# Kernel tuning notes

Hardware: AMD Instinct MI355X
Metric: run time of the kernel (lower is better)

The kernel has to match this reference:

```python
import jax, jax.numpy as jnp
import numpy as np

R = 2.0            # distance exponent
Q = 1.0            # activation exponent
SPECIFICITY = 1.0  # c in exp(-c * dist)
BETA = 3.0         # lateral competition exponent
TEMP_COMP = 1.0    # ClusterCompetition temperature
TEMP_WTA = 0.1     # SoftWTA temperature
PHI = 1.5          # association scaling
NEG_INF = -1e30

B, C, D = 1024, 512, 256


def setup_inputs() -> dict:
    key = jax.random.key(0)
    k1, k2, k3, k4, k5 = jax.random.split(key, 5)
    inp = jax.random.normal(k1, (B, D), dtype=jnp.float32)
    w_dist = jax.random.normal(k2, (C, D), dtype=jnp.float32)      # cluster centers
    attn = jax.random.uniform(k3, (D,), dtype=jnp.float32)         # dim-wise attention (>=0)
    w_assoc = jax.random.normal(k4, (C, 2), dtype=jnp.float32)     # association weights
    mask = jax.random.randint(k5, (C,), 0, 2, dtype=jnp.int32)     # recruited-cluster mask
    return {"inp": inp, "w_dist": w_dist, "attn": attn, "w_assoc": w_assoc, "mask": mask}


def reference(inp, w_dist, attn, w_assoc, mask):
    m = mask.astype(inp.dtype)                       # [C] 0/1 recruited gate
    # Distance: per-dim |x - w|^r for every (item, cluster) pair -> [B, C, D]
    dim_dist = jnp.abs(inp[:, None, :] - w_dist[None, :, :]) ** R
    # DimWiseAttention: sum-to-one constrained attention over dims
    a = attn / jnp.sum(attn)
    # ClusterActivation: H_j = exp(-c * (sum_d a_d * dist_d)^(q/r)) -> [B, C]
    wdist = jnp.einsum('bcd,d->bc', dim_dist, a)
    H = jnp.exp(-SPECIFICITY * wdist ** (Q / R))
    clusters_actv = H * m                            # MaskNonRecruit
    nonzero = m > 0
    # ClusterCompetition: softmax over recruited clusters of actv^beta (temp-scaled),
    # re-weighting each cluster's own activation.
    comp_logits = jnp.where(nonzero, BETA * jnp.log(H) / TEMP_COMP, NEG_INF)
    p_comp = jax.nn.softmax(comp_logits, axis=-1)
    competed = p_comp * clusters_actv                # [B, C]
    # SoftWTA: plain temperature softmax over recruited clusters, same re-weighting.
    wta_logits = jnp.where(nonzero, competed / TEMP_WTA, NEG_INF)
    p_wta = jax.nn.softmax(wta_logits, axis=-1)
    softwta = p_wta * competed                       # [B, C]
    # Classification: Phi-scaled linear readout to 2 classes.
    y_pred = PHI * (softwta @ w_assoc)               # [B, 2]
    return y_pred
```

## Files before the change

### kernel.cpp

```cpp
#include <hip/hip_runtime.h>
#include <math.h>

#define BN 1024
#define CN 512
#define DN 256
#define TM 128
#define TN 64
#define KZ 32
#define NZ (DN / KZ)

#define XS_OFF 0
#define R_OFF  (BN * DN)
#define Q_OFF  (R_OFF + BN)
#define PD_OFF (Q_OFF + CN)

__launch_bounds__(256, 4)
__global__ void prep_kernel(const float* __restrict__ inp, const float* __restrict__ wd,
                            const float* __restrict__ attn, float* __restrict__ ws) {
    __shared__ float red[4];
    float* xs = ws + XS_OFF;
    float* r  = ws + R_OFF;
    float* q  = ws + Q_OFF;

    const int tid  = threadIdx.x;
    const int lane = tid & 63;
    const int blk  = blockIdx.x;

    float av = attn[tid];
    float s = av;
    #pragma unroll
    for (int off = 32; off > 0; off >>= 1) s += __shfl_xor(s, off);
    if (lane == 0) red[tid >> 6] = s;
    __syncthreads();
    const float a = av / (red[0] + red[1] + red[2] + red[3]);

    float c;
    if (blk < BN) {
        const float x = inp[blk * DN + tid];
        xs[blk * DN + tid] = a * x;
        c = a * x * x;
    } else {
        const float w = wd[(blk - BN) * DN + tid];
        c = a * w * w;
    }
    #pragma unroll
    for (int off = 32; off > 0; off >>= 1) c += __shfl_xor(c, off);
    __syncthreads();
    if (lane == 0) red[tid >> 6] = c;
    __syncthreads();
    if (tid == 0) {
        const float tot = red[0] + red[1] + red[2] + red[3];
        if (blk < BN) r[blk] = tot; else q[blk - BN] = tot;
    }
}

__launch_bounds__(256, 2)
__global__ void dist_kernel(const float* __restrict__ ws_ro, const float* __restrict__ wd,
                            float* __restrict__ ws) {
    __shared__ __align__(16) float aT[TM * KZ];
    __shared__ __align__(16) float bT[TN * KZ];

    const float* xs = ws_ro + XS_OFF;
    float* pdot = ws + PD_OFF + (size_t)blockIdx.z * BN * CN;

    const int tid = threadIdx.x;
    const int m0 = blockIdx.x * TM;
    const int n0 = blockIdx.y * TN;
    const int k0 = blockIdx.z * KZ;

    {
        const int row = tid >> 1;
        const int g0  = (tid & 1) * 4;
        const int sw  = (row >> 3) & 7;
        const float* src = &xs[(m0 + row) * DN + k0 + 4 * g0];
        float4* dst = (float4*)&aT[row * KZ];
        #pragma unroll
        for (int j = 0; j < 4; ++j)
            dst[(g0 + j) ^ sw] = *(const float4*)&src[4 * j];
    }
    {
        const int row = tid >> 2;
        const int g0  = (tid & 3) * 2;
        const int sw  = (row >> 3) & 7;
        const float* src = &wd[(n0 + row) * DN + k0 + 4 * g0];
        float4* dst = (float4*)&bT[row * KZ];
        #pragma unroll
        for (int j = 0; j < 2; ++j)
            dst[(g0 + j) ^ sw] = *(const float4*)&src[4 * j];
    }
    __syncthreads();

    const int tr = tid & 15;
    const int tc = tid >> 4;
    const int swa = tr & 7;
    const int swb = (tc >> 1) & 7;
    float acc[8][4] = {};

    #pragma unroll
    for (int k4 = 0; k4 < KZ / 4; ++k4) {
        float4 av[8], bv[4];
        #pragma unroll
        for (int i = 0; i < 8; ++i)
            av[i] = ((const float4*)&aT[(8 * tr + i) * KZ])[k4 ^ swa];
        #pragma unroll
        for (int j = 0; j < 4; ++j)
            bv[j] = ((const float4*)&bT[(4 * tc + j) * KZ])[k4 ^ swb];
        #pragma unroll
        for (int i = 0; i < 8; ++i)
            #pragma unroll
            for (int j = 0; j < 4; ++j) {
                float t = fmaf(av[i].x, bv[j].x, acc[i][j]);
                t = fmaf(av[i].y, bv[j].y, t);
                t = fmaf(av[i].z, bv[j].z, t);
                acc[i][j] = fmaf(av[i].w, bv[j].w, t);
            }
    }

    #pragma unroll
    for (int i = 0; i < 8; ++i) {
        float4 o = {acc[i][0], acc[i][1], acc[i][2], acc[i][3]};
        *(float4*)&pdot[(m0 + 8 * tr + i) * CN + n0 + 4 * tc] = o;
    }
}

#define NEG_INF_F (-1e30f)

__device__ __forceinline__ float waveMax(float v) {
    #pragma unroll
    for (int off = 32; off > 0; off >>= 1) v = fmaxf(v, __shfl_xor(v, off));
    return v;
}
__device__ __forceinline__ float waveSum(float v) {
    #pragma unroll
    for (int off = 32; off > 0; off >>= 1) v += __shfl_xor(v, off);
    return v;
}

__launch_bounds__(256, 2)
__global__ void finish_kernel(const float* __restrict__ ws, const int* __restrict__ mask,
                              const float* __restrict__ w_assoc, float* __restrict__ y) {
    const float* r    = ws + R_OFF;
    const float* q    = ws + Q_OFF;
    const float* pdot = ws + PD_OFF;

    const int tid  = threadIdx.x;
    const int lane = tid & 63;
    const int b    = blockIdx.x * 4 + (tid >> 6);
    const int cb   = lane * 8;

    float dot[8] = {};
    #pragma unroll
    for (int z = 0; z < NZ; ++z) {
        const float* pz = &pdot[(size_t)z * BN * CN + b * CN + cb];
        #pragma unroll
        for (int s4 = 0; s4 < 2; ++s4) {
            const float4 v = *(const float4*)&pz[4 * s4];
            dot[4 * s4 + 0] += v.x; dot[4 * s4 + 1] += v.y;
            dot[4 * s4 + 2] += v.z; dot[4 * s4 + 3] += v.w;
        }
    }
    const float rb = r[b];
    const float4 q0 = *(const float4*)&q[cb];
    const float4 q1 = *(const float4*)&q[cb + 4];
    const float qv[8] = {q0.x, q0.y, q0.z, q0.w, q1.x, q1.y, q1.z, q1.w};

    float t[8];
    #pragma unroll
    for (int j = 0; j < 8; ++j)
        t[j] = sqrtf(fmaxf(rb + qv[j] - 2.0f * dot[j], 0.0f));

    const int4 mm0 = *(const int4*)&mask[cb];
    const int4 mm1 = *(const int4*)&mask[cb + 4];
    const bool rec[8] = {mm0.x > 0, mm0.y > 0, mm0.z > 0, mm0.w > 0,
                         mm1.x > 0, mm1.y > 0, mm1.z > 0, mm1.w > 0};

    float l1[8], lmax = NEG_INF_F;
    #pragma unroll
    for (int j = 0; j < 8; ++j) { l1[j] = rec[j] ? (-3.0f * t[j]) : NEG_INF_F; lmax = fmaxf(lmax, l1[j]); }
    const float mx1 = waveMax(lmax);
    float e1[8], lsum = 0.f;
    #pragma unroll
    for (int j = 0; j < 8; ++j) { e1[j] = rec[j] ? expf(l1[j] - mx1) : 0.f; lsum += e1[j]; }
    const float inv_s1 = 1.0f / waveSum(lsum);

    float competed[8];
    #pragma unroll
    for (int j = 0; j < 8; ++j) competed[j] = e1[j] * inv_s1 * expf(-t[j]);

    float l2[8]; lmax = NEG_INF_F;
    #pragma unroll
    for (int j = 0; j < 8; ++j) { l2[j] = rec[j] ? (competed[j] * 10.0f) : NEG_INF_F; lmax = fmaxf(lmax, l2[j]); }
    const float mx2 = waveMax(lmax);
    float e2[8]; lsum = 0.f;
    #pragma unroll
    for (int j = 0; j < 8; ++j) { e2[j] = rec[j] ? expf(l2[j] - mx2) : 0.f; lsum += e2[j]; }
    const float inv_s2 = 1.0f / waveSum(lsum);

    float y0 = 0.f, y1 = 0.f;
    #pragma unroll
    for (int p = 0; p < 4; ++p) {
        const float4 wa = *(const float4*)&w_assoc[2 * cb + 4 * p];
        const float sw0 = e2[2 * p + 0] * inv_s2 * competed[2 * p + 0];
        const float sw1 = e2[2 * p + 1] * inv_s2 * competed[2 * p + 1];
        y0 = fmaf(sw0, wa.x, y0); y1 = fmaf(sw0, wa.y, y1);
        y0 = fmaf(sw1, wa.z, y0); y1 = fmaf(sw1, wa.w, y1);
    }
    y0 = waveSum(y0);
    y1 = waveSum(y1);
    if (lane == 0) {
        float2 o = {1.5f * y0, 1.5f * y1};
        *(float2*)&y[b * 2] = o;
    }
}

extern "C" void kernel_launch(void* const* d_in, const int* in_sizes, int n_in,
                              void* d_out, int out_size, void* d_ws, size_t ws_size,
                              hipStream_t stream) {
    const float* inp     = (const float*)d_in[0];
    const float* w_dist  = (const float*)d_in[1];
    const float* attn    = (const float*)d_in[2];
    const float* w_assoc = (const float*)d_in[3];
    const int*   mask    = (const int*)d_in[4];
    float* out = (float*)d_out;
    float* ws  = (float*)d_ws;

    prep_kernel<<<BN + CN, 256, 0, stream>>>(inp, w_dist, attn, ws);
    dim3 gA(BN / TM, CN / TN, NZ);
    dist_kernel<<<gA, 256, 0, stream>>>(ws, w_dist, ws);
    finish_kernel<<<BN / 4, 256, 0, stream>>>(ws, mask, w_assoc, out);
}
```

Before: 82.94 us.

## Fuse distance GEMM and softmax readout into one kernel with in-block k-split reduction

Replaces the tiled split-K dist kernel, which wrote 8 partial dot-product planes to global workspace, and the separate finish kernel with a single fused kernel. Each 512-thread block handles 4 batch rows. Each wave computes a K-slice of the dot products against all 512 clusters, reading w_dist straight from global memory. The partials are reduced in shared memory and the softmax readout runs in place. This removes the large partial-sum round trip and one launch, but gives up LDS tiling: w_dist is re-read from global/L2 by every block, with strided per-lane accesses and low data reuse.

```diff
diff --git a/kernel.cpp b/kernel.cpp
--- a/kernel.cpp
+++ b/kernel.cpp
@@ -4,15 +4,13 @@
 #define BN 1024
 #define CN 512
 #define DN 256
-#define TM 128
-#define TN 64
-#define KZ 32
-#define NZ (DN / KZ)
+#define ROWS 4
+#define WAVES 8
+#define KC (DN / WAVES)
 
 #define XS_OFF 0
 #define R_OFF  (BN * DN)
 #define Q_OFF  (R_OFF + BN)
-#define PD_OFF (Q_OFF + CN)
 
 __launch_bounds__(256, 4)
 __global__ void prep_kernel(const float* __restrict__ inp, const float* __restrict__ wd,
@@ -54,75 +52,6 @@
     }
 }
 
-__launch_bounds__(256, 2)
-__global__ void dist_kernel(const float* __restrict__ ws_ro, const float* __restrict__ wd,
-                            float* __restrict__ ws) {
-    __shared__ __align__(16) float aT[TM * KZ];
-    __shared__ __align__(16) float bT[TN * KZ];
-
-    const float* xs = ws_ro + XS_OFF;
-    float* pdot = ws + PD_OFF + (size_t)blockIdx.z * BN * CN;
-
-    const int tid = threadIdx.x;
-    const int m0 = blockIdx.x * TM;
-    const int n0 = blockIdx.y * TN;
-    const int k0 = blockIdx.z * KZ;
-
-    {
-        const int row = tid >> 1;
-        const int g0  = (tid & 1) * 4;
-        const int sw  = (row >> 3) & 7;
-        const float* src = &xs[(m0 + row) * DN + k0 + 4 * g0];
-        float4* dst = (float4*)&aT[row * KZ];
-        #pragma unroll
-        for (int j = 0; j < 4; ++j)
-            dst[(g0 + j) ^ sw] = *(const float4*)&src[4 * j];
-    }
-    {
-        const int row = tid >> 2;
-        const int g0  = (tid & 3) * 2;
-        const int sw  = (row >> 3) & 7;
-        const float* src = &wd[(n0 + row) * DN + k0 + 4 * g0];
-        float4* dst = (float4*)&bT[row * KZ];
-        #pragma unroll
-        for (int j = 0; j < 2; ++j)
-            dst[(g0 + j) ^ sw] = *(const float4*)&src[4 * j];
-    }
-    __syncthreads();
-
-    const int tr = tid & 15;
-    const int tc = tid >> 4;
-    const int swa = tr & 7;
-    const int swb = (tc >> 1) & 7;
-    float acc[8][4] = {};
-
-    #pragma unroll
-    for (int k4 = 0; k4 < KZ / 4; ++k4) {
-        float4 av[8], bv[4];
-        #pragma unroll
-        for (int i = 0; i < 8; ++i)
-            av[i] = ((const float4*)&aT[(8 * tr + i) * KZ])[k4 ^ swa];
-        #pragma unroll
-        for (int j = 0; j < 4; ++j)
-            bv[j] = ((const float4*)&bT[(4 * tc + j) * KZ])[k4 ^ swb];
-        #pragma unroll
-        for (int i = 0; i < 8; ++i)
-            #pragma unroll
-            for (int j = 0; j < 4; ++j) {
-                float t = fmaf(av[i].x, bv[j].x, acc[i][j]);
-                t = fmaf(av[i].y, bv[j].y, t);
-                t = fmaf(av[i].z, bv[j].z, t);
-                acc[i][j] = fmaf(av[i].w, bv[j].w, t);
-            }
-    }
-
-    #pragma unroll
-    for (int i = 0; i < 8; ++i) {
-        float4 o = {acc[i][0], acc[i][1], acc[i][2], acc[i][3]};
-        *(float4*)&pdot[(m0 + 8 * tr + i) * CN + n0 + 4 * tc] = o;
-    }
-}
-
 #define NEG_INF_F (-1e30f)
 
 __device__ __forceinline__ float waveMax(float v) {
@@ -136,80 +65,113 @@
     return v;
 }
 
-__launch_bounds__(256, 2)
-__global__ void finish_kernel(const float* __restrict__ ws, const int* __restrict__ mask,
-                              const float* __restrict__ w_assoc, float* __restrict__ y) {
-    const float* r    = ws + R_OFF;
-    const float* q    = ws + Q_OFF;
-    const float* pdot = ws + PD_OFF;
+__launch_bounds__(512, 1)
+__global__ void fused_kernel(const float* __restrict__ ws, const float* __restrict__ wd,
+                             const int* __restrict__ mask, const float* __restrict__ w_assoc,
+                             float* __restrict__ y) {
+    __shared__ float red[WAVES * 32 * 64];
 
     const int tid  = threadIdx.x;
     const int lane = tid & 63;
-    const int b    = blockIdx.x * 4 + (tid >> 6);
-    const int cb   = lane * 8;
+    const int wz   = __builtin_amdgcn_readfirstlane(tid >> 6);
+    const int b0   = blockIdx.x * ROWS;
+    const int kbase = wz * KC;
 
-    float dot[8] = {};
+    const float* xs = ws + XS_OFF;
+
+    const float* wp[8];
     #pragma unroll
-    for (int z = 0; z < NZ; ++z) {
-        const float* pz = &pdot[(size_t)z * BN * CN + b * CN + cb];
+    for (int j = 0; j < 8; ++j)
+        wp[j] = wd + (size_t)(lane + 64 * j) * DN + kbase;
+
+    float acc[ROWS][8] = {};
+
+    #pragma unroll
+    for (int k4 = 0; k4 < KC / 4; ++k4) {
+        float4 xv[ROWS];
         #pragma unroll
-        for (int s4 = 0; s4 < 2; ++s4) {
-            const float4 v = *(const float4*)&pz[4 * s4];
-            dot[4 * s4 + 0] += v.x; dot[4 * s4 + 1] += v.y;
-            dot[4 * s4 + 2] += v.z; dot[4 * s4 + 3] += v.w;
+        for (int rr = 0; rr < ROWS; ++rr) {
+            const int idx = __builtin_amdgcn_readfirstlane((b0 + rr) * DN + kbase + 4 * k4);
+            xv[rr] = *(const float4*)&xs[idx];
+        }
+        #pragma unroll
+        for (int j = 0; j < 8; ++j) {
+            const float4 w4 = *(const float4*)(wp[j] + 4 * k4);
+            #pragma unroll
+            for (int rr = 0; rr < ROWS; ++rr) {
+                float t = fmaf(xv[rr].x, w4.x, acc[rr][j]);
+                t = fmaf(xv[rr].y, w4.y, t);
+                t = fmaf(xv[rr].z, w4.z, t);
+                acc[rr][j] = fmaf(xv[rr].w, w4.w, t);
+            }
         }
     }
-    const float rb = r[b];
-    const float4 q0 = *(const float4*)&q[cb];
-    const float4 q1 = *(const float4*)&q[cb + 4];
-    const float qv[8] = {q0.x, q0.y, q0.z, q0.w, q1.x, q1.y, q1.z, q1.w};
 
-    float t[8];
     #pragma unroll
-    for (int j = 0; j < 8; ++j)
-        t[j] = sqrtf(fmaxf(rb + qv[j] - 2.0f * dot[j], 0.0f));
+    for (int rr = 0; rr < ROWS; ++rr)
+        #pragma unroll
+        for (int j = 0; j < 8; ++j)
+            red[(wz * 32 + rr * 8 + j) * 64 + lane] = acc[rr][j];
+    __syncthreads();
 
-    const int4 mm0 = *(const int4*)&mask[cb];
-    const int4 mm1 = *(const int4*)&mask[cb + 4];
-    const bool rec[8] = {mm0.x > 0, mm0.y > 0, mm0.z > 0, mm0.w > 0,
-                         mm1.x > 0, mm1.y > 0, mm1.z > 0, mm1.w > 0};
+    if (wz < ROWS) {
+        const int rr = wz;
 
-    float l1[8], lmax = NEG_INF_F;
-    #pragma unroll
-    for (int j = 0; j < 8; ++j) { l1[j] = rec[j] ? (-3.0f * t[j]) : NEG_INF_F; lmax = fmaxf(lmax, l1[j]); }
-    const float mx1 = waveMax(lmax);
-    float e1[8], lsum = 0.f;
-    #pragma unroll
-    for (int j = 0; j < 8; ++j) { e1[j] = rec[j] ? expf(l1[j] - mx1) : 0.f; lsum += e1[j]; }
-    const float inv_s1 = 1.0f / waveSum(lsum);
+        float dot[8] = {};
+        #pragma unroll
+        for (int z = 0; z < WAVES; ++z)
+            #pragma unroll
+            for (int j = 0; j < 8; ++j)
+                dot[j] += red[(z * 32 + rr * 8 + j) * 64 + lane];
 
-    float competed[8];
-    #pragma unroll
-    for (int j = 0; j < 8; ++j) competed[j] = e1[j] * inv_s1 * expf(-t[j]);
+        const float rb = ws[R_OFF + b0 + rr];
 
-    float l2[8]; lmax = NEG_INF_F;
-    #pragma unroll
-    for (int j = 0; j < 8; ++j) { l2[j] = rec[j] ? (competed[j] * 10.0f) : NEG_INF_F; lmax = fmaxf(lmax, l2[j]); }
-    const float mx2 = waveMax(lmax);
-    float e2[8]; lsum = 0.f;
-    #pragma unroll
-    for (int j = 0; j < 8; ++j) { e2[j] = rec[j] ? expf(l2[j] - mx2) : 0.f; lsum += e2[j]; }
-    const float inv_s2 = 1.0f / waveSum(lsum);
+        float t[8]; bool rec[8];
+        #pragma unroll
+        for (int j = 0; j < 8; ++j) {
+            const int c = lane + 64 * j;
+            const float wdist = fmaxf(rb + ws[Q_OFF + c] - 2.0f * dot[j], 0.0f);
+            t[j] = sqrtf(wdist);
+            rec[j] = mask[c] > 0;
+        }
 
-    float y0 = 0.f, y1 = 0.f;
-    #pragma unroll
-    for (int p = 0; p < 4; ++p) {
-        const float4 wa = *(const float4*)&w_assoc[2 * cb + 4 * p];
-        const float sw0 = e2[2 * p + 0] * inv_s2 * competed[2 * p + 0];
-        const float sw1 = e2[2 * p + 1] * inv_s2 * competed[2 * p + 1];
-        y0 = fmaf(sw0, wa.x, y0); y1 = fmaf(sw0, wa.y, y1);
-        y0 = fmaf(sw1, wa.z, y0); y1 = fmaf(sw1, wa.w, y1);
-    }
-    y0 = waveSum(y0);
-    y1 = waveSum(y1);
-    if (lane == 0) {
-        float2 o = {1.5f * y0, 1.5f * y1};
-        *(float2*)&y[b * 2] = o;
+        float l1[8], lmax = NEG_INF_F;
+        #pragma unroll
+        for (int j = 0; j < 8; ++j) { l1[j] = rec[j] ? (-3.0f * t[j]) : NEG_INF_F; lmax = fmaxf(lmax, l1[j]); }
+        const float mx1 = waveMax(lmax);
+        float e1[8], lsum = 0.f;
+        #pragma unroll
+        for (int j = 0; j < 8; ++j) { e1[j] = rec[j] ? expf(l1[j] - mx1) : 0.f; lsum += e1[j]; }
+        const float inv_s1 = 1.0f / waveSum(lsum);
+
+        float competed[8];
+        #pragma unroll
+        for (int j = 0; j < 8; ++j) competed[j] = e1[j] * inv_s1 * expf(-t[j]);
+
+        float l2[8]; lmax = NEG_INF_F;
+        #pragma unroll
+        for (int j = 0; j < 8; ++j) { l2[j] = rec[j] ? (competed[j] * 10.0f) : NEG_INF_F; lmax = fmaxf(lmax, l2[j]); }
+        const float mx2 = waveMax(lmax);
+        float e2[8]; lsum = 0.f;
+        #pragma unroll
+        for (int j = 0; j < 8; ++j) { e2[j] = rec[j] ? expf(l2[j] - mx2) : 0.f; lsum += e2[j]; }
+        const float inv_s2 = 1.0f / waveSum(lsum);
+
+        float y0 = 0.f, y1 = 0.f;
+        #pragma unroll
+        for (int j = 0; j < 8; ++j) {
+            const int c = lane + 64 * j;
+            const float sw = e2[j] * inv_s2 * competed[j];
+            const float2 wa = *(const float2*)&w_assoc[2 * c];
+            y0 = fmaf(sw, wa.x, y0);
+            y1 = fmaf(sw, wa.y, y1);
+        }
+        y0 = waveSum(y0);
+        y1 = waveSum(y1);
+        if (lane == 0) {
+            float2 o = {1.5f * y0, 1.5f * y1};
+            *(float2*)&y[(b0 + rr) * 2] = o;
+        }
     }
 }
 
@@ -225,7 +187,5 @@
     float* ws  = (float*)d_ws;
 
     prep_kernel<<<BN + CN, 256, 0, stream>>>(inp, w_dist, attn, ws);
-    dim3 gA(BN / TM, CN / TN, NZ);
-    dist_kernel<<<gA, 256, 0, stream>>>(ws, w_dist, ws);
-    finish_kernel<<<BN / 4, 256, 0, stream>>>(ws, mask, w_assoc, out);
+    fused_kernel<<<BN / ROWS, 512, 0, stream>>>(ws, w_dist, mask, w_assoc, out);
 }
```

New measurement: 87.83 us. 5.9% more time.
